# Optimization experiments

Measured on AMD Instinct MI355X. Metric: run time of the kernel, lower is better.

Reference implementation:

```python
import jax, jax.numpy as jnp
import numpy as np

SEQ_LEN = 96      # args.seq_len (in_feats)
H_FEATS = 100
OUT_FEATS = 128
HEADS = 4
K = 64            # args.input_size = nodes per graph
B = 256           # number of graphs (batch_size)
N = K * B
DEG = 8
E = N * DEG
OUT_SIZE = 24     # args.output_size
NEG_SLOPE = 0.2   # PyG GATConv default


def setup_inputs() -> dict:
    key = jax.random.key(0)
    ks = jax.random.split(key, 20)
    s = 0.05
    x = jax.random.normal(ks[0], (N, SEQ_LEN), jnp.float32)
    # intra-graph random edges (dst repeated, src within same graph)
    dst = jnp.repeat(jnp.arange(N, dtype=jnp.int32), DEG)
    src = (dst // K) * K + jax.random.randint(ks[1], (E,), 0, K, dtype=jnp.int32)
    edge_index = jnp.stack([src, dst])
    batch = jnp.repeat(jnp.arange(B, dtype=jnp.int32), K)
    y = jax.random.normal(ks[2], (N, OUT_SIZE), jnp.float32)
    # GATConv 1: in=96 -> heads=4, ch=100
    W1 = jax.random.normal(ks[3], (SEQ_LEN, HEADS * H_FEATS), jnp.float32) * s
    as1 = jax.random.normal(ks[4], (HEADS, H_FEATS), jnp.float32) * s
    ad1 = jax.random.normal(ks[5], (HEADS, H_FEATS), jnp.float32) * s
    b1 = jnp.zeros((H_FEATS,), jnp.float32)
    # GATConv 2: in=100 -> heads=4, ch=128
    W2 = jax.random.normal(ks[6], (H_FEATS, HEADS * OUT_FEATS), jnp.float32) * s
    as2 = jax.random.normal(ks[7], (HEADS, OUT_FEATS), jnp.float32) * s
    ad2 = jax.random.normal(ks[8], (HEADS, OUT_FEATS), jnp.float32) * s
    b2 = jnp.zeros((OUT_FEATS,), jnp.float32)
    # per-node-index MLPs (batched over K)
    fw1 = jax.random.normal(ks[9], (K, OUT_FEATS, 64), jnp.float32) * s
    fb1 = jnp.zeros((K, 64), jnp.float32)
    fw2 = jax.random.normal(ks[10], (K, 64, OUT_SIZE), jnp.float32) * s
    fb2 = jnp.zeros((K, OUT_SIZE), jnp.float32)
    return dict(x=x, edge_index=edge_index, batch=batch, y=y,
                W1=W1, as1=as1, ad1=ad1, b1=b1,
                W2=W2, as2=as2, ad2=ad2, b2=b2,
                fw1=fw1, fb1=fb1, fw2=fw2, fb2=fb2)


def gat_conv(x, src, dst, W, a_src, a_dst, bias):
    # PyG GATConv (concat=False): linear -> per-edge attention -> softmax over
    # incoming edges of each dst -> weighted sum -> mean over heads + bias.
    n = x.shape[0]
    xl = (x @ W).reshape(n, HEADS, -1)                      # [N,H,C]
    al_src = jnp.sum(xl * a_src, axis=-1)                   # [N,H]
    al_dst = jnp.sum(xl * a_dst, axis=-1)                   # [N,H]
    alpha = jax.nn.leaky_relu(al_src[src] + al_dst[dst], NEG_SLOPE)  # [E,H]
    m = jax.ops.segment_max(alpha, dst, num_segments=n)
    ea = jnp.exp(alpha - m[dst])
    denom = jax.ops.segment_sum(ea, dst, num_segments=n)
    w = ea / (denom[dst] + 1e-16)                           # [E,H]
    msg = xl[src] * w[:, :, None]                           # [E,H,C]
    out = jax.ops.segment_sum(msg, dst, num_segments=n)     # [N,H,C]
    return out.mean(axis=1) + bias                          # concat=False


def reference(x, edge_index, batch, y, W1, as1, ad1, b1, W2, as2, ad2, b2, fw1, fb1, fw2, fb2):
    n = x.shape[0]
    src, dst = edge_index[0], edge_index[1]
    loop = jnp.arange(n, dtype=src.dtype)                   # GATConv adds self-loops
    src = jnp.concatenate([src, loop])
    dst = jnp.concatenate([dst, loop])
    h = jax.nn.elu(gat_conv(x, src, dst, W1, as1, ad1, b1))
    h = gat_conv(h, src, dst, W2, as2, ad2, b2)             # [N,128]
    # batch is sorted with K nodes per graph -> stacking == static reshape
    xg = h.reshape(B, K, OUT_FEATS).transpose(1, 0, 2)      # [K,B,128]
    hid = jax.nn.relu(jnp.einsum('kbi,kih->kbh', xg, fw1) + fb1[:, None, :])
    pred = jnp.einsum('kbh,kho->kbo', hid, fw2) + fb2[:, None, :]  # [K,B,out]
    yg = y.reshape(B, K, OUT_SIZE)                          # [B,K,out]
    return pred, yg
```

## Files before the change

### kernel.cpp

```cpp
#include <hip/hip_runtime.h>
#include <hip/hip_bf16.h>
#include <math.h>


#define N_NODES 16384
#define B_GRAPHS 256
#define K_NODES 64
#define DEG 8
#define NHEADS 4
#define C1 100
#define C2 128
#define IN_F 96
#define HID 64
#define OUT_SZ 24
#define PRED_ELEMS (K_NODES * B_GRAPHS * OUT_SZ)

#define W1T_ROWS 448
#define W1T_K    96
#define W2T_ROWS 512
#define W2T_K    128

using bf16 = __hip_bfloat16;
typedef __attribute__((ext_vector_type(8))) short          frag_ab;
typedef __attribute__((ext_vector_type(4))) float          frag_cd;
typedef unsigned short us8 __attribute__((ext_vector_type(8)));
typedef unsigned short us4 __attribute__((ext_vector_type(4)));

__device__ __forceinline__ float us2f(unsigned short u) {
  return __bfloat162float(__ushort_as_bfloat16(u));
}
__device__ __forceinline__ short f2bf_s(float f) {
  return __builtin_bit_cast(short, __float2bfloat16(f));
}

#define P1N (W1T_ROWS * W1T_K)
#define P2N (W2T_ROWS * W2T_K)
#define YG4 (PRED_ELEMS / 4)

__global__ __launch_bounds__(256)
void prep(const float* __restrict__ W1, const float* __restrict__ W2,
          const float* __restrict__ y,
          bf16* __restrict__ W1t, bf16* __restrict__ W2t,
          float* __restrict__ yg) {
  int idx = blockIdx.x * 256 + threadIdx.x;
  if (idx < P1N) {
    int c = idx / W1T_K, k = idx - c * W1T_K;
    W1t[idx] = __float2bfloat16((c < 400) ? W1[(size_t)k * 400 + c] : 0.f);
  } else if (idx < P1N + P2N) {
    int i2 = idx - P1N;
    int c = i2 >> 7, k = i2 & 127;
    W2t[i2] = __float2bfloat16((k < 100) ? W2[(size_t)k * 512 + c] : 0.f);
  } else {
    int j = idx - P1N - P2N;
    if (j < YG4) {
      int i = j * 4;
      float4 v = *(const float4*)(y + i);
      v.x = __bfloat162float(__float2bfloat16(v.x));
      v.y = __bfloat162float(__float2bfloat16(v.y));
      v.z = __bfloat162float(__float2bfloat16(v.z));
      v.w = __bfloat162float(__float2bfloat16(v.w));
      *(float4*)(yg + i) = v;
    }
  }
}

__global__ __launch_bounds__(512)
void gat_fused(const float* __restrict__ x,
               const bf16* __restrict__ W1t, const bf16* __restrict__ W2t,
               const int* __restrict__ esrc,
               const float* __restrict__ as1, const float* __restrict__ ad1,
               const float* __restrict__ b1,
               const float* __restrict__ as2, const float* __restrict__ ad2,
               const float* __restrict__ b2,
               bf16* __restrict__ h2out) {
  constexpr int LDA1 = IN_F + 8;
  constexpr int LDA2 = 136;
  constexpr int LDT  = 72;

  __shared__ __align__(16) short          As[64 * LDA2];
  __shared__ __align__(16) unsigned short xs[512 * LDT];
  __shared__ __align__(16) short          Ps[NHEADS * 64 * LDT];
  __shared__ float avs1[400], avd1[400], avs2[512], avd2[512];
  __shared__ float bia1[C1], bia2[C2];
  __shared__ int   edg[K_NODES * DEG];
  __shared__ float als[64 * 5], ald[64 * 5];

  const int g = blockIdx.x;
  const int t = threadIdx.x;
  const int wv = t >> 6;
  const int l  = t & 63;
  const int lm = l & 15;
  const int lk = (l >> 4) * 8;
  const int rq = (l >> 4) * 4;

  {
    constexpr int QR = IN_F / 4;
    for (int idx = t; idx < 64 * QR; idx += 512) {
      int m = idx / QR, q = idx - m * QR;
      const float4 v = *(const float4*)(x + ((size_t)(g * 64 + m) * IN_F + q * 4));
      short* d = &As[m * LDA1 + q * 4];
      d[0] = f2bf_s(v.x); d[1] = f2bf_s(v.y); d[2] = f2bf_s(v.z); d[3] = f2bf_s(v.w);
    }
  }
  for (int idx = t; idx < 400; idx += 512) { avs1[idx] = as1[idx]; avd1[idx] = ad1[idx]; }
  for (int idx = t; idx < 512; idx += 512) { avs2[idx] = as2[idx]; avd2[idx] = ad2[idx]; }
  if (t < C1) bia1[t] = b1[t];
  if (t < C2) bia2[t] = b2[t];
  if (t < K_NODES * DEG) edg[t] = esrc[g * K_NODES * DEG + t] & (K_NODES - 1);
  for (int idx = t; idx < NHEADS * 64 * LDT / 8; idx += 512)
    *(us8*)&Ps[idx * 8] = (us8)0;
  __syncthreads();

  if (wv < 7) {
    const int n0 = wv * 64;
    frag_cd acc[4][4] = {};
#pragma unroll
    for (int ks = 0; ks < IN_F; ks += 32) {
      frag_ab b[4];
#pragma unroll
      for (int nt = 0; nt < 4; ++nt)
        b[nt] = *(const frag_ab*)((const short*)W1t +
                                  (size_t)(n0 + nt * 16 + lm) * W1T_K + ks + lk);
#pragma unroll
      for (int mt = 0; mt < 4; ++mt) {
        frag_ab a = *(const frag_ab*)&As[(mt * 16 + lm) * LDA1 + ks + lk];
#pragma unroll
        for (int nt = 0; nt < 4; ++nt)
          acc[mt][nt] = __builtin_amdgcn_mfma_f32_16x16x32_bf16(a, b[nt],
                                                                acc[mt][nt], 0, 0, 0);
      }
    }
#pragma unroll
    for (int mt = 0; mt < 4; ++mt)
#pragma unroll
      for (int nt = 0; nt < 4; ++nt) {
        const int c4 = n0 + nt * 16 + lm;
        us4 o;
#pragma unroll
        for (int r = 0; r < 4; ++r) o[r] = (unsigned short)f2bf_s(acc[mt][nt][r]);
        *(us4*)&xs[c4 * LDT + mt * 16 + rq] = o;
      }
  }
  __syncthreads();

  if (t < 256) {
    const int n = t >> 2, h = t & 3;
    float ss = 0.f, sd = 0.f;
#pragma unroll 4
    for (int c = 0; c < C1; ++c) {
      const float v = us2f(xs[(h * C1 + c) * LDT + n]);
      ss += v * avs1[h * C1 + c];
      sd += v * avd1[h * C1 + c];
    }
    als[n * 5 + h] = ss;
    ald[n * 5 + h] = sd;
  }
  __syncthreads();

  if (t < 256) {
    const int n = t >> 2, h = t & 3;
    const float ad = ald[n * 5 + h];
    int   sv[9];
    float a[9];
#pragma unroll
    for (int j = 0; j < 8; ++j) sv[j] = edg[n * DEG + j];
    sv[8] = n;
#pragma unroll
    for (int j = 0; j < 9; ++j) {
      float v = als[sv[j] * 5 + h] + ad;
      a[j] = (v >= 0.f) ? v : 0.2f * v;
    }
    float m = -1e30f;
#pragma unroll
    for (int j = 0; j < 9; ++j) m = fmaxf(m, a[j]);
    float s = 0.f;
#pragma unroll
    for (int j = 0; j < 9; ++j) { a[j] = __expf(a[j] - m); s += a[j]; }
    const float inv = 1.f / (s + 1e-16f);
    short* prow = &Ps[(h * 64 + n) * LDT];
#pragma unroll
    for (int j = 0; j < 9; ++j) {
      float tw = a[j];
#pragma unroll
      for (int i = 0; i < 9; ++i)
        if (i != j && sv[i] == sv[j]) tw += a[i];
      prow[sv[j]] = f2bf_s(tw * inv);
    }
  } else {
    for (int i = t - 256; i < 64 * 28; i += 256) {
      int m = i / 28, kk = 100 + (i - m * 28);
      As[m * LDA2 + kk] = 0;
    }
  }
  __syncthreads();

  {
    const int mw = (wv & 3) * 16;
    const int cg = wv >> 2;
    const int ntb = cg * 4;
    const int nte = (cg == 0) ? 4 : 7;
    frag_cd acc[4] = {};
#pragma unroll
    for (int h = 0; h < NHEADS; ++h)
#pragma unroll
      for (int ks = 0; ks < 64; ks += 32) {
        frag_ab a = *(const frag_ab*)&Ps[(h * 64 + mw + lm) * LDT + ks + lk];
        for (int nt = ntb; nt < nte; ++nt) {
          frag_ab b = *(const frag_ab*)&xs[(h * C1 + nt * 16 + lm) * LDT + ks + lk];
          acc[nt - ntb] = __builtin_amdgcn_mfma_f32_16x16x32_bf16(a, b,
                                                                  acc[nt - ntb], 0, 0, 0);
      }
    }
    for (int nt = ntb; nt < nte; ++nt) {
      const int c = nt * 16 + lm;
      if (c < C1) {
        const float bc = bia1[c];
#pragma unroll
        for (int r = 0; r < 4; ++r) {
          float vv = acc[nt - ntb][r] * 0.25f + bc;
          vv = (vv > 0.f) ? vv : (__expf(vv) - 1.f);
          As[(mw + rq + r) * LDA2 + c] = f2bf_s(vv);
        }
      }
    }
  }
  __syncthreads();

  {
    const int n0 = wv * 64;
    frag_cd acc[4][4] = {};
#pragma unroll
    for (int ks = 0; ks < 128; ks += 32) {
      frag_ab b[4];
#pragma unroll
      for (int nt = 0; nt < 4; ++nt)
        b[nt] = *(const frag_ab*)((const short*)W2t +
                                  (size_t)(n0 + nt * 16 + lm) * W2T_K + ks + lk);
#pragma unroll
      for (int mt = 0; mt < 4; ++mt) {
        frag_ab a = *(const frag_ab*)&As[(mt * 16 + lm) * LDA2 + ks + lk];
#pragma unroll
        for (int nt = 0; nt < 4; ++nt)
          acc[mt][nt] = __builtin_amdgcn_mfma_f32_16x16x32_bf16(a, b[nt],
                                                                acc[mt][nt], 0, 0, 0);
      }
    }
#pragma unroll
    for (int mt = 0; mt < 4; ++mt)
#pragma unroll
      for (int nt = 0; nt < 4; ++nt) {
        const int c4 = n0 + nt * 16 + lm;
        us4 o;
#pragma unroll
        for (int r = 0; r < 4; ++r) o[r] = (unsigned short)f2bf_s(acc[mt][nt][r]);
        *(us4*)&xs[c4 * LDT + mt * 16 + rq] = o;
      }
  }
  __syncthreads();

  if (t < 256) {
    const int n = t >> 2, h = t & 3;
    float ss = 0.f, sd = 0.f;
#pragma unroll 4
    for (int c = 0; c < C2; ++c) {
      const float v = us2f(xs[(h * C2 + c) * LDT + n]);
      ss += v * avs2[h * C2 + c];
      sd += v * avd2[h * C2 + c];
    }
    als[n * 5 + h] = ss;
    ald[n * 5 + h] = sd;
  }
  __syncthreads();

  if (t < 256) {
    const int n = t >> 2, h = t & 3;
    const float ad = ald[n * 5 + h];
    int   sv[9];
    float a[9];
#pragma unroll
    for (int j = 0; j < 8; ++j) sv[j] = edg[n * DEG + j];
    sv[8] = n;
#pragma unroll
    for (int j = 0; j < 9; ++j) {
      float v = als[sv[j] * 5 + h] + ad;
      a[j] = (v >= 0.f) ? v : 0.2f * v;
    }
    float m = -1e30f;
#pragma unroll
    for (int j = 0; j < 9; ++j) m = fmaxf(m, a[j]);
    float s = 0.f;
#pragma unroll
    for (int j = 0; j < 9; ++j) { a[j] = __expf(a[j] - m); s += a[j]; }
    const float inv = 1.f / (s + 1e-16f);
    short* prow = &Ps[(h * 64 + n) * LDT];
#pragma unroll
    for (int j = 0; j < 9; ++j) {
      float tw = a[j];
#pragma unroll
      for (int i = 0; i < 9; ++i)
        if (i != j && sv[i] == sv[j]) tw += a[i];
      prow[sv[j]] = f2bf_s(tw * inv);
    }
  }
  __syncthreads();

  {
    const int mw = (wv & 3) * 16;
    const int cg = wv >> 2;
    const int ntb = cg * 4;
    frag_cd acc[4] = {};
#pragma unroll
    for (int h = 0; h < NHEADS; ++h)
#pragma unroll
      for (int ks = 0; ks < 64; ks += 32) {
        frag_ab a = *(const frag_ab*)&Ps[(h * 64 + mw + lm) * LDT + ks + lk];
#pragma unroll
        for (int nt = 0; nt < 4; ++nt) {
          frag_ab b = *(const frag_ab*)&xs[(h * C2 + (ntb + nt) * 16 + lm) * LDT + ks + lk];
          acc[nt] = __builtin_amdgcn_mfma_f32_16x16x32_bf16(a, b, acc[nt], 0, 0, 0);
        }
      }
    unsigned short* outp = (unsigned short*)h2out + (size_t)(g * 64) * C2;
#pragma unroll
    for (int nt = 0; nt < 4; ++nt) {
      const int c = (ntb + nt) * 16 + lm;
      const float bc = bia2[c];
#pragma unroll
      for (int r = 0; r < 4; ++r) {
        float vv = acc[nt][r] * 0.25f + bc;
        outp[(size_t)(mw + rq + r) * C2 + c] = (unsigned short)f2bf_s(vv);
      }
    }
  }
}

__global__ __launch_bounds__(256)
void mlp_mfma(const bf16* __restrict__ h2,
              const float* __restrict__ fw1, const float* __restrict__ fb1,
              const float* __restrict__ fw2, const float* __restrict__ fb2,
              float* __restrict__ pred) {
  constexpr int LDA = C2 + 8;
  constexpr int LDH = HID + 8;
  __shared__ __align__(16) short As[64 * LDA];
  __shared__ __align__(16) short B1[HID * LDA];
  __shared__ __align__(16) short Hs[64 * LDH];
  __shared__ __align__(16) short B2[32 * LDH];
  __shared__ float b1s[HID];
  __shared__ float b2s[32];

  const int k  = blockIdx.x & 63;
  const int ms = blockIdx.x >> 6;
  const int t  = threadIdx.x;

  for (int idx = t; idx < 64 * 16; idx += 256) {
    int r = idx >> 4, o = idx & 15;
    const us8 v = *(const us8*)((const unsigned short*)h2 +
        ((size_t)((ms * 64 + r) * K_NODES + k) * C2) + o * 8);
    *(us8*)&As[r * LDA + o * 8] = v;
  }
  for (int idx = t; idx < C2 * HID; idx += 256) {
    int kk = idx >> 6, n = idx & 63;
    B1[n * LDA + kk] = f2bf_s(fw1[(size_t)k * C2 * HID + kk * HID + n]);
  }
  for (int idx = t; idx < HID * 32; idx += 256) {
    int kk = idx >> 5, n = idx & 31;
    float v = (n < OUT_SZ) ? fw2[(size_t)k * HID * OUT_SZ + kk * OUT_SZ + n] : 0.f;
    B2[n * LDH + kk] = f2bf_s(v);
  }
  if (t < HID) b1s[t] = fb1[k * HID + t];
  if (t < 32)  b2s[t] = (t < OUT_SZ) ? fb2[k * OUT_SZ + t] : 0.f;
  __syncthreads();

  const int wv = t >> 6;
  const int l  = t & 63;
  const int lm = l & 15;
  const int lk = (l >> 4) * 8;
  const int rq = (l >> 4) * 4;

  frag_cd acc[4] = {};
#pragma unroll
  for (int ks = 0; ks < C2; ks += 32) {
    frag_ab a = *(const frag_ab*)&As[(wv * 16 + lm) * LDA + ks + lk];
#pragma unroll
    for (int nt = 0; nt < 4; ++nt) {
      frag_ab b = *(const frag_ab*)&B1[(nt * 16 + lm) * LDA + ks + lk];
      acc[nt] = __builtin_amdgcn_mfma_f32_16x16x32_bf16(a, b, acc[nt], 0, 0, 0);
    }
  }
#pragma unroll
  for (int nt = 0; nt < 4; ++nt) {
    const int j  = nt * 16 + lm;
    const float bj = b1s[j];
#pragma unroll
    for (int r = 0; r < 4; ++r) {
      const int m = wv * 16 + rq + r;
      Hs[m * LDH + j] = f2bf_s(fmaxf(acc[nt][r] + bj, 0.f));
    }
  }
  __syncthreads();

  frag_cd acc2[2] = {};
#pragma unroll
  for (int ks = 0; ks < HID; ks += 32) {
    frag_ab a = *(const frag_ab*)&Hs[(wv * 16 + lm) * LDH + ks + lk];
#pragma unroll
    for (int nt = 0; nt < 2; ++nt) {
      frag_ab b = *(const frag_ab*)&B2[(nt * 16 + lm) * LDH + ks + lk];
      acc2[nt] = __builtin_amdgcn_mfma_f32_16x16x32_bf16(a, b, acc2[nt], 0, 0, 0);
    }
  }
#pragma unroll
  for (int nt = 0; nt < 2; ++nt) {
    const int q = nt * 16 + lm;
    if (q < OUT_SZ) {
      const float bq = b2s[q];
#pragma unroll
      for (int r = 0; r < 4; ++r) {
        const int m = wv * 16 + rq + r;
        pred[((size_t)k * B_GRAPHS + ms * 64 + m) * OUT_SZ + q] = acc2[nt][r] + bq;
      }
    }
  }
}

extern "C" void kernel_launch(void* const* d_in, const int* in_sizes, int n_in,
                              void* d_out, int out_size, void* d_ws, size_t ws_size,
                              hipStream_t stream) {
  const float* x   = (const float*)d_in[0];
  const int*   ei  = (const int*)d_in[1];
  const float* y   = (const float*)d_in[3];
  const float* W1  = (const float*)d_in[4];
  const float* as1 = (const float*)d_in[5];
  const float* ad1 = (const float*)d_in[6];
  const float* b1  = (const float*)d_in[7];
  const float* W2  = (const float*)d_in[8];
  const float* as2 = (const float*)d_in[9];
  const float* ad2 = (const float*)d_in[10];
  const float* b2  = (const float*)d_in[11];
  const float* fw1 = (const float*)d_in[12];
  const float* fb1 = (const float*)d_in[13];
  const float* fw2 = (const float*)d_in[14];
  const float* fb2 = (const float*)d_in[15];

  bf16* h2  = (bf16*)d_ws;
  bf16* W1t = h2 + (size_t)N_NODES * C2;
  bf16* W2t = W1t + P1N;

  float* out = (float*)d_out;

  prep<<<(P1N + P2N + YG4 + 255) / 256, 256, 0, stream>>>(
      W1, W2, y, W1t, W2t, out + PRED_ELEMS);

  gat_fused<<<B_GRAPHS, 512, 0, stream>>>(x, W1t, W2t, ei,
                                          as1, ad1, b1, as2, ad2, b2, h2);

  mlp_mfma<<<K_NODES * 4, 256, 0, stream>>>(h2, fw1, fb1, fw2, fb2, out);
}
```

Before: 118.6 us.

## Fold attention vectors into weights, overlap logit compute, pretranspose MLP weights

Precomputes W·a_src/W·a_dst in the prep kernel so attention logits come straight from the layer input, computed by the spare wave while the other waves run the GEMM. This removes a barrier and the strided reads of xs. The softmax step is spread across all eight waves instead of half the block. The MLP weights are converted to transposed bf16 once in prep so mlp_mfma loads them with vector copies, and mlp_mfma now launches twice as many blocks with half the rows each. The cost is a larger prep kernel with serial dot-product threads, and logits computed from bf16 inputs with fp32 weight products, which rounds slightly differently.

```diff
diff --git a/kernel.cpp b/kernel.cpp
--- a/kernel.cpp
+++ b/kernel.cpp
@@ -20,6 +20,14 @@
 #define W2T_ROWS 512
 #define W2T_K    128
 
+#define P1N (W1T_ROWS * W1T_K)
+#define P2N (W2T_ROWS * W2T_K)
+#define F1N (K_NODES * HID * C2)
+#define F2N (K_NODES * 32 * HID)
+#define YG4 (PRED_ELEMS / 4)
+#define WAN (768 + 1024)
+#define PREPN (P1N + P2N + F1N + F2N + YG4 + WAN)
+
 using bf16 = __hip_bfloat16;
 typedef __attribute__((ext_vector_type(8))) short          frag_ab;
 typedef __attribute__((ext_vector_type(4))) float          frag_cd;
@@ -33,15 +41,17 @@
   return __builtin_bit_cast(short, __float2bfloat16(f));
 }
 
-#define P1N (W1T_ROWS * W1T_K)
-#define P2N (W2T_ROWS * W2T_K)
-#define YG4 (PRED_ELEMS / 4)
-
 __global__ __launch_bounds__(256)
 void prep(const float* __restrict__ W1, const float* __restrict__ W2,
+          const float* __restrict__ fw1, const float* __restrict__ fw2,
           const float* __restrict__ y,
+          const float* __restrict__ as1, const float* __restrict__ ad1,
+          const float* __restrict__ as2, const float* __restrict__ ad2,
           bf16* __restrict__ W1t, bf16* __restrict__ W2t,
-          float* __restrict__ yg) {
+          bf16* __restrict__ fw1t, bf16* __restrict__ fw2t,
+          float* __restrict__ yg,
+          float* __restrict__ wa1s, float* __restrict__ wa1d,
+          float* __restrict__ wa2s, float* __restrict__ wa2d) {
   int idx = blockIdx.x * 256 + threadIdx.x;
   if (idx < P1N) {
     int c = idx / W1T_K, k = idx - c * W1T_K;
@@ -50,16 +60,42 @@
     int i2 = idx - P1N;
     int c = i2 >> 7, k = i2 & 127;
     W2t[i2] = __float2bfloat16((k < 100) ? W2[(size_t)k * 512 + c] : 0.f);
+  } else if (idx < P1N + P2N + F1N) {
+    int i2 = idx - P1N - P2N;
+    int k = i2 >> 13, r = i2 & 8191, j = r >> 7, i = r & 127;
+    fw1t[i2] = __float2bfloat16(fw1[(size_t)k * 8192 + i * 64 + j]);
+  } else if (idx < P1N + P2N + F1N + F2N) {
+    int i2 = idx - P1N - P2N - F1N;
+    int k = i2 >> 11, r = i2 & 2047, q = r >> 6, j = r & 63;
+    fw2t[i2] = __float2bfloat16((q < OUT_SZ) ? fw2[(size_t)k * 1536 + j * 24 + q] : 0.f);
+  } else if (idx < P1N + P2N + F1N + F2N + YG4) {
+    int j = idx - P1N - P2N - F1N - F2N;
+    int i = j * 4;
+    float4 v = *(const float4*)(y + i);
+    v.x = __bfloat162float(__float2bfloat16(v.x));
+    v.y = __bfloat162float(__float2bfloat16(v.y));
+    v.z = __bfloat162float(__float2bfloat16(v.z));
+    v.w = __bfloat162float(__float2bfloat16(v.w));
+    *(float4*)(yg + i) = v;
   } else {
-    int j = idx - P1N - P2N;
-    if (j < YG4) {
-      int i = j * 4;
-      float4 v = *(const float4*)(y + i);
-      v.x = __bfloat162float(__float2bfloat16(v.x));
-      v.y = __bfloat162float(__float2bfloat16(v.y));
-      v.z = __bfloat162float(__float2bfloat16(v.z));
-      v.w = __bfloat162float(__float2bfloat16(v.w));
-      *(float4*)(yg + i) = v;
+    int tw = idx - P1N - P2N - F1N - F2N - YG4;
+    if (tw < 768) {
+      int k = tw >> 3, h = (tw >> 1) & 3, sd = tw & 1;
+      const float* a = sd ? ad1 : as1;
+      float s = 0.f;
+      for (int c = 0; c < C1; ++c)
+        s += W1[(size_t)k * 400 + h * C1 + c] * a[h * C1 + c];
+      (sd ? wa1d : wa1s)[k * 4 + h] = s;
+    } else if (tw < WAN) {
+      int t2 = tw - 768;
+      int k = t2 >> 3, h = (t2 >> 1) & 3, sd = t2 & 1;
+      float s = 0.f;
+      if (k < 100) {
+        const float* a = sd ? ad2 : as2;
+        for (int c = 0; c < C2; ++c)
+          s += W2[(size_t)k * 512 + h * C2 + c] * a[h * C2 + c];
+      }
+      (sd ? wa2d : wa2s)[k * 4 + h] = s;
     }
   }
 }
@@ -68,10 +104,9 @@
 void gat_fused(const float* __restrict__ x,
                const bf16* __restrict__ W1t, const bf16* __restrict__ W2t,
                const int* __restrict__ esrc,
-               const float* __restrict__ as1, const float* __restrict__ ad1,
-               const float* __restrict__ b1,
-               const float* __restrict__ as2, const float* __restrict__ ad2,
-               const float* __restrict__ b2,
+               const float* __restrict__ wa1s_g, const float* __restrict__ wa1d_g,
+               const float* __restrict__ wa2s_g, const float* __restrict__ wa2d_g,
+               const float* __restrict__ b1, const float* __restrict__ b2,
                bf16* __restrict__ h2out) {
   constexpr int LDA1 = IN_F + 8;
   constexpr int LDA2 = 136;
@@ -80,7 +115,7 @@
   __shared__ __align__(16) short          As[64 * LDA2];
   __shared__ __align__(16) unsigned short xs[512 * LDT];
   __shared__ __align__(16) short          Ps[NHEADS * 64 * LDT];
-  __shared__ float avs1[400], avd1[400], avs2[512], avd2[512];
+  __shared__ float wa1s[384], wa1d[384], wa2s[512], wa2d[512];
   __shared__ float bia1[C1], bia2[C2];
   __shared__ int   edg[K_NODES * DEG];
   __shared__ float als[64 * 5], ald[64 * 5];
@@ -102,11 +137,11 @@
       d[0] = f2bf_s(v.x); d[1] = f2bf_s(v.y); d[2] = f2bf_s(v.z); d[3] = f2bf_s(v.w);
     }
   }
-  for (int idx = t; idx < 400; idx += 512) { avs1[idx] = as1[idx]; avd1[idx] = ad1[idx]; }
-  for (int idx = t; idx < 512; idx += 512) { avs2[idx] = as2[idx]; avd2[idx] = ad2[idx]; }
+  if (t < 384) { wa1s[t] = wa1s_g[t]; wa1d[t] = wa1d_g[t]; }
+  { wa2s[t] = wa2s_g[t]; wa2d[t] = wa2d_g[t]; }
   if (t < C1) bia1[t] = b1[t];
-  if (t < C2) bia2[t] = b2[t];
-  if (t < K_NODES * DEG) edg[t] = esrc[g * K_NODES * DEG + t] & (K_NODES - 1);
+  if (t >= 128 && t < 128 + C2) bia2[t - 128] = b2[t - 128];
+  edg[t] = esrc[g * K_NODES * DEG + t] & (K_NODES - 1);
   for (int idx = t; idx < NHEADS * 64 * LDT / 8; idx += 512)
     *(us8*)&Ps[idx * 8] = (us8)0;
   __syncthreads();
@@ -140,65 +175,69 @@
         for (int r = 0; r < 4; ++r) o[r] = (unsigned short)f2bf_s(acc[mt][nt][r]);
         *(us4*)&xs[c4 * LDT + mt * 16 + rq] = o;
       }
-  }
-  __syncthreads();
-
-  if (t < 256) {
-    const int n = t >> 2, h = t & 3;
-    float ss = 0.f, sd = 0.f;
-#pragma unroll 4
-    for (int c = 0; c < C1; ++c) {
-      const float v = us2f(xs[(h * C1 + c) * LDT + n]);
-      ss += v * avs1[h * C1 + c];
-      sd += v * avd1[h * C1 + c];
-    }
-    als[n * 5 + h] = ss;
-    ald[n * 5 + h] = sd;
-  }
-  __syncthreads();
-
-  if (t < 256) {
-    const int n = t >> 2, h = t & 3;
-    const float ad = ald[n * 5 + h];
-    int   sv[9];
-    float a[9];
-#pragma unroll
-    for (int j = 0; j < 8; ++j) sv[j] = edg[n * DEG + j];
-    sv[8] = n;
-#pragma unroll
-    for (int j = 0; j < 9; ++j) {
-      float v = als[sv[j] * 5 + h] + ad;
-      a[j] = (v >= 0.f) ? v : 0.2f * v;
-    }
-    float m = -1e30f;
-#pragma unroll
-    for (int j = 0; j < 9; ++j) m = fmaxf(m, a[j]);
-    float s = 0.f;
-#pragma unroll
-    for (int j = 0; j < 9; ++j) { a[j] = __expf(a[j] - m); s += a[j]; }
-    const float inv = 1.f / (s + 1e-16f);
-    short* prow = &Ps[(h * 64 + n) * LDT];
-#pragma unroll
-    for (int j = 0; j < 9; ++j) {
-      float tw = a[j];
-#pragma unroll
-      for (int i = 0; i < 9; ++i)
-        if (i != j && sv[i] == sv[j]) tw += a[i];
-      prow[sv[j]] = f2bf_s(tw * inv);
-    }
   } else {
-    for (int i = t - 256; i < 64 * 28; i += 256) {
-      int m = i / 28, kk = 100 + (i - m * 28);
-      As[m * LDA2 + kk] = 0;
-    }
+    const int n = l;
+    float ss[4] = {}, dd[4] = {};
+#pragma unroll
+    for (int o = 0; o < IN_F / 8; ++o) {
+      const us8 v = *(const us8*)&((const unsigned short*)As)[n * LDA1 + o * 8];
+#pragma unroll
+      for (int j = 0; j < 8; ++j) {
+        const float f = us2f(v[j]);
+        const int k4 = (o * 8 + j) * 4;
+#pragma unroll
+        for (int h = 0; h < 4; ++h) {
+          ss[h] += f * wa1s[k4 + h];
+          dd[h] += f * wa1d[k4 + h];
+        }
+      }
+    }
+#pragma unroll
+    for (int h = 0; h < 4; ++h) { als[n * 5 + h] = ss[h]; ald[n * 5 + h] = dd[h]; }
   }
   __syncthreads();
 
   {
     const int mw = (wv & 3) * 16;
-    const int cg = wv >> 2;
-    const int ntb = cg * 4;
-    const int nte = (cg == 0) ? 4 : 7;
+    {
+      const int n = mw + (l >> 2), h = l & 3;
+      const float ad = ald[n * 5 + h];
+      int   sv[9];
+      float a[9];
+#pragma unroll
+      for (int j = 0; j < 8; ++j) sv[j] = edg[n * DEG + j];
+      sv[8] = n;
+#pragma unroll
+      for (int j = 0; j < 9; ++j) {
+        float v = als[sv[j] * 5 + h] + ad;
+        a[j] = (v >= 0.f) ? v : 0.2f * v;
+      }
+      float m = -1e30f;
+#pragma unroll
+      for (int j = 0; j < 9; ++j) m = fmaxf(m, a[j]);
+      float s = 0.f;
+#pragma unroll
+      for (int j = 0; j < 9; ++j) { a[j] = __expf(a[j] - m); s += a[j]; }
+      const float inv = 1.f / (s + 1e-16f);
+      short* prow = &Ps[(h * 64 + n) * LDT];
+#pragma unroll
+      for (int j = 0; j < 9; ++j) {
+        float tw = a[j];
+#pragma unroll
+        for (int i = 0; i < 9; ++i)
+          if (i != j && sv[i] == sv[j]) tw += a[i];
+        prow[sv[j]] = f2bf_s(tw * inv);
+      }
+    }
+    if (wv >= 4) {
+      for (int i = (wv - 4) * 64 + l; i < 64 * 28; i += 256) {
+        int m = i / 28, kk = 100 + (i - m * 28);
+        As[m * LDA2 + kk] = 0;
+      }
+    }
+    const int cgi = wv >> 2;
+    const int ntb = cgi * 4;
+    const int nte = (cgi == 0) ? 4 : 7;
     frag_cd acc[4] = {};
 #pragma unroll
     for (int h = 0; h < NHEADS; ++h)
@@ -209,8 +248,8 @@
           frag_ab b = *(const frag_ab*)&xs[(h * C1 + nt * 16 + lm) * LDT + ks + lk];
           acc[nt - ntb] = __builtin_amdgcn_mfma_f32_16x16x32_bf16(a, b,
                                                                   acc[nt - ntb], 0, 0, 0);
-      }
-    }
+        }
+      }
     for (int nt = ntb; nt < nte; ++nt) {
       const int c = nt * 16 + lm;
       if (c < C1) {
@@ -255,59 +294,56 @@
         for (int r = 0; r < 4; ++r) o[r] = (unsigned short)f2bf_s(acc[mt][nt][r]);
         *(us4*)&xs[c4 * LDT + mt * 16 + rq] = o;
       }
-  }
-  __syncthreads();
-
-  if (t < 256) {
-    const int n = t >> 2, h = t & 3;
-    float ss = 0.f, sd = 0.f;
-#pragma unroll 4
-    for (int c = 0; c < C2; ++c) {
-      const float v = us2f(xs[(h * C2 + c) * LDT + n]);
-      ss += v * avs2[h * C2 + c];
-      sd += v * avd2[h * C2 + c];
-    }
-    als[n * 5 + h] = ss;
-    ald[n * 5 + h] = sd;
-  }
-  __syncthreads();
-
-  if (t < 256) {
-    const int n = t >> 2, h = t & 3;
-    const float ad = ald[n * 5 + h];
-    int   sv[9];
-    float a[9];
-#pragma unroll
-    for (int j = 0; j < 8; ++j) sv[j] = edg[n * DEG + j];
-    sv[8] = n;
-#pragma unroll
-    for (int j = 0; j < 9; ++j) {
-      float v = als[sv[j] * 5 + h] + ad;
-      a[j] = (v >= 0.f) ? v : 0.2f * v;
-    }
-    float m = -1e30f;
-#pragma unroll
-    for (int j = 0; j < 9; ++j) m = fmaxf(m, a[j]);
+    const int n  = wv * 8 + (l >> 3);
+    const int h  = (l >> 1) & 3;
+    const int sd = l & 1;
+    const float* wa = sd ? wa2d : wa2s;
     float s = 0.f;
 #pragma unroll
-    for (int j = 0; j < 9; ++j) { a[j] = __expf(a[j] - m); s += a[j]; }
-    const float inv = 1.f / (s + 1e-16f);
-    short* prow = &Ps[(h * 64 + n) * LDT];
-#pragma unroll
-    for (int j = 0; j < 9; ++j) {
-      float tw = a[j];
-#pragma unroll
-      for (int i = 0; i < 9; ++i)
-        if (i != j && sv[i] == sv[j]) tw += a[i];
-      prow[sv[j]] = f2bf_s(tw * inv);
-    }
+    for (int o = 0; o < 16; ++o) {
+      const us8 v = *(const us8*)&((const unsigned short*)As)[n * LDA2 + o * 8];
+#pragma unroll
+      for (int j = 0; j < 8; ++j)
+        s += us2f(v[j]) * wa[(o * 8 + j) * 4 + h];
+    }
+    if (sd) ald[n * 5 + h] = s; else als[n * 5 + h] = s;
   }
   __syncthreads();
 
   {
     const int mw = (wv & 3) * 16;
-    const int cg = wv >> 2;
-    const int ntb = cg * 4;
+    {
+      const int n = mw + (l >> 2), h = l & 3;
+      const float ad = ald[n * 5 + h];
+      int   sv[9];
+      float a[9];
+#pragma unroll
+      for (int j = 0; j < 8; ++j) sv[j] = edg[n * DEG + j];
+      sv[8] = n;
+#pragma unroll
+      for (int j = 0; j < 9; ++j) {
+        float v = als[sv[j] * 5 + h] + ad;
+        a[j] = (v >= 0.f) ? v : 0.2f * v;
+      }
+      float m = -1e30f;
+#pragma unroll
+      for (int j = 0; j < 9; ++j) m = fmaxf(m, a[j]);
+      float s = 0.f;
+#pragma unroll
+      for (int j = 0; j < 9; ++j) { a[j] = __expf(a[j] - m); s += a[j]; }
+      const float inv = 1.f / (s + 1e-16f);
+      short* prow = &Ps[(h * 64 + n) * LDT];
+#pragma unroll
+      for (int j = 0; j < 9; ++j) {
+        float tw = a[j];
+#pragma unroll
+        for (int i = 0; i < 9; ++i)
+          if (i != j && sv[i] == sv[j]) tw += a[i];
+        prow[sv[j]] = f2bf_s(tw * inv);
+      }
+    }
+    const int cgi = wv >> 2;
+    const int ntb = cgi * 4;
     frag_cd acc[4] = {};
 #pragma unroll
     for (int h = 0; h < NHEADS; ++h)
@@ -336,14 +372,14 @@
 
 __global__ __launch_bounds__(256)
 void mlp_mfma(const bf16* __restrict__ h2,
-              const float* __restrict__ fw1, const float* __restrict__ fb1,
-              const float* __restrict__ fw2, const float* __restrict__ fb2,
+              const bf16* __restrict__ fw1t, const float* __restrict__ fb1,
+              const bf16* __restrict__ fw2t, const float* __restrict__ fb2,
               float* __restrict__ pred) {
-  constexpr int LDA = C2 + 8;
-  constexpr int LDH = HID + 8;
-  __shared__ __align__(16) short As[64 * LDA];
+  constexpr int LDA = 136;
+  constexpr int LDH = 72;
+  __shared__ __align__(16) short As[32 * LDA];
   __shared__ __align__(16) short B1[HID * LDA];
-  __shared__ __align__(16) short Hs[64 * LDH];
+  __shared__ __align__(16) short Hs[32 * LDH];
   __shared__ __align__(16) short B2[32 * LDH];
   __shared__ float b1s[HID];
   __shared__ float b2s[32];
@@ -352,23 +388,24 @@
   const int ms = blockIdx.x >> 6;
   const int t  = threadIdx.x;
 
-  for (int idx = t; idx < 64 * 16; idx += 256) {
+  for (int idx = t; idx < 32 * 16; idx += 256) {
     int r = idx >> 4, o = idx & 15;
     const us8 v = *(const us8*)((const unsigned short*)h2 +
-        ((size_t)((ms * 64 + r) * K_NODES + k) * C2) + o * 8);
+        ((size_t)((ms * 32 + r) * K_NODES + k) * C2) + o * 8);
     *(us8*)&As[r * LDA + o * 8] = v;
   }
-  for (int idx = t; idx < C2 * HID; idx += 256) {
-    int kk = idx >> 6, n = idx & 63;
-    B1[n * LDA + kk] = f2bf_s(fw1[(size_t)k * C2 * HID + kk * HID + n]);
-  }
-  for (int idx = t; idx < HID * 32; idx += 256) {
-    int kk = idx >> 5, n = idx & 31;
-    float v = (n < OUT_SZ) ? fw2[(size_t)k * HID * OUT_SZ + kk * OUT_SZ + n] : 0.f;
-    B2[n * LDH + kk] = f2bf_s(v);
+  for (int idx = t; idx < HID * 16; idx += 256) {
+    int n = idx >> 4, o = idx & 15;
+    *(us8*)&B1[n * LDA + o * 8] =
+        *(const us8*)((const unsigned short*)fw1t + (size_t)k * 8192 + n * 128 + o * 8);
+  }
+  for (int idx = t; idx < 32 * 8; idx += 256) {
+    int q = idx >> 3, o = idx & 7;
+    *(us8*)&B2[q * LDH + o * 8] =
+        *(const us8*)((const unsigned short*)fw2t + (size_t)k * 2048 + q * 64 + o * 8);
   }
   if (t < HID) b1s[t] = fb1[k * HID + t];
-  if (t < 32)  b2s[t] = (t < OUT_SZ) ? fb2[k * OUT_SZ + t] : 0.f;
+  if (t >= 64 && t < 96) b2s[t - 64] = (t - 64 < OUT_SZ) ? fb2[k * OUT_SZ + (t - 64)] : 0.f;
   __syncthreads();
 
   const int wv = t >> 6;
@@ -377,48 +414,46 @@
   const int lk = (l >> 4) * 8;
   const int rq = (l >> 4) * 4;
 
-  frag_cd acc[4] = {};
-#pragma unroll
-  for (int ks = 0; ks < C2; ks += 32) {
-    frag_ab a = *(const frag_ab*)&As[(wv * 16 + lm) * LDA + ks + lk];
-#pragma unroll
-    for (int nt = 0; nt < 4; ++nt) {
-      frag_ab b = *(const frag_ab*)&B1[(nt * 16 + lm) * LDA + ks + lk];
-      acc[nt] = __builtin_amdgcn_mfma_f32_16x16x32_bf16(a, b, acc[nt], 0, 0, 0);
-    }
-  }
-#pragma unroll
-  for (int nt = 0; nt < 4; ++nt) {
-    const int j  = nt * 16 + lm;
-    const float bj = b1s[j];
-#pragma unroll
-    for (int r = 0; r < 4; ++r) {
-      const int m = wv * 16 + rq + r;
-      Hs[m * LDH + j] = f2bf_s(fmaxf(acc[nt][r] + bj, 0.f));
+  {
+    const int mt  = wv & 1;
+    const int ntp = wv >> 1;
+    frag_cd acc[2] = {};
+#pragma unroll
+    for (int ks = 0; ks < C2; ks += 32) {
+      frag_ab a = *(const frag_ab*)&As[(mt * 16 + lm) * LDA + ks + lk];
+#pragma unroll
+      for (int u = 0; u < 2; ++u) {
+        frag_ab b = *(const frag_ab*)&B1[((ntp * 2 + u) * 16 + lm) * LDA + ks + lk];
+        acc[u] = __builtin_amdgcn_mfma_f32_16x16x32_bf16(a, b, acc[u], 0, 0, 0);
+      }
+    }
+#pragma unroll
+    for (int u = 0; u < 2; ++u) {
+      const int j  = (ntp * 2 + u) * 16 + lm;
+      const float bj = b1s[j];
+#pragma unroll
+      for (int r = 0; r < 4; ++r)
+        Hs[(mt * 16 + rq + r) * LDH + j] = f2bf_s(fmaxf(acc[u][r] + bj, 0.f));
     }
   }
   __syncthreads();
 
-  frag_cd acc2[2] = {};
-#pragma unroll
-  for (int ks = 0; ks < HID; ks += 32) {
-    frag_ab a = *(const frag_ab*)&Hs[(wv * 16 + lm) * LDH + ks + lk];
-#pragma unroll
-    for (int nt = 0; nt < 2; ++nt) {
+  {
+    const int mt = wv >> 1;
+    const int nt = wv & 1;
+    frag_cd acc = {};
+#pragma unroll
+    for (int ks = 0; ks < HID; ks += 32) {
+      frag_ab a = *(const frag_ab*)&Hs[(mt * 16 + lm) * LDH + ks + lk];
       frag_ab b = *(const frag_ab*)&B2[(nt * 16 + lm) * LDH + ks + lk];
-      acc2[nt] = __builtin_amdgcn_mfma_f32_16x16x32_bf16(a, b, acc2[nt], 0, 0, 0);
-    }
-  }
-#pragma unroll
-  for (int nt = 0; nt < 2; ++nt) {
+      acc = __builtin_amdgcn_mfma_f32_16x16x32_bf16(a, b, acc, 0, 0, 0);
+    }
     const int q = nt * 16 + lm;
     if (q < OUT_SZ) {
       const float bq = b2s[q];
 #pragma unroll
-      for (int r = 0; r < 4; ++r) {
-        const int m = wv * 16 + rq + r;
-        pred[((size_t)k * B_GRAPHS + ms * 64 + m) * OUT_SZ + q] = acc2[nt][r] + bq;
-      }
+      for (int r = 0; r < 4; ++r)
+        pred[((size_t)k * B_GRAPHS + ms * 32 + mt * 16 + rq + r) * OUT_SZ + q] = acc[r] + bq;
     }
   }
 }
@@ -442,17 +477,24 @@
   const float* fw2 = (const float*)d_in[14];
   const float* fb2 = (const float*)d_in[15];
 
-  bf16* h2  = (bf16*)d_ws;
-  bf16* W1t = h2 + (size_t)N_NODES * C2;
-  bf16* W2t = W1t + P1N;
+  bf16* h2    = (bf16*)d_ws;
+  bf16* W1t   = h2 + (size_t)N_NODES * C2;
+  bf16* W2t   = W1t + P1N;
+  bf16* fw1t  = W2t + P2N;
+  bf16* fw2t  = fw1t + F1N;
+  float* wa1s = (float*)(fw2t + F2N);
+  float* wa1d = wa1s + 384;
+  float* wa2s = wa1d + 384;
+  float* wa2d = wa2s + 512;
 
   float* out = (float*)d_out;
 
-  prep<<<(P1N + P2N + YG4 + 255) / 256, 256, 0, stream>>>(
-      W1, W2, y, W1t, W2t, out + PRED_ELEMS);
+  prep<<<(PREPN + 255) / 256, 256, 0, stream>>>(
+      W1, W2, fw1, fw2, y, as1, ad1, as2, ad2,
+      W1t, W2t, fw1t, fw2t, out + PRED_ELEMS, wa1s, wa1d, wa2s, wa2d);
 
   gat_fused<<<B_GRAPHS, 512, 0, stream>>>(x, W1t, W2t, ei,
-                                          as1, ad1, b1, as2, ad2, b2, h2);
-
-  mlp_mfma<<<K_NODES * 4, 256, 0, stream>>>(h2, fw1, fb1, fw2, fb2, out);
+                                          wa1s, wa1d, wa2s, wa2d, b1, b2, h2);
+
+  mlp_mfma<<<K_NODES * 8, 256, 0, stream>>>(h2, fw1t, fb1, fw2t, fb2, out);
 }
```

New measurement: 123.1 us. +3.8%, slower.
